# Kernel optimization log

Measured on AMD Instinct MI355X. Metric: run time of the kernel, lower is better.

## Reference

```python
import jax, jax.numpy as jnp
import numpy as np

BETA = 0.25  # commitment_cost


def setup_inputs() -> dict:
    key = jax.random.key(0)
    k1, k2 = jax.random.split(key)
    z = jax.random.normal(k1, (16, 4096, 256), dtype=jnp.float32)
    embed_w = jax.random.normal(k2, (2048, 256), dtype=jnp.float32)
    return {"z": z, "embed_w": embed_w}


def reference(z, embed_w):
    K, D = embed_w.shape
    zf = z.reshape(-1, D)                                   # [N, D]
    N = zf.shape[0]
    # squared euclidean distances: ||z||^2 + ||e||^2 - 2 z e^T  -> [N, K]
    d = (jnp.sum(zf * zf, axis=1, keepdims=True)
         + jnp.sum(embed_w * embed_w, axis=1)
         - 2.0 * jnp.matmul(zf, embed_w.T))
    encoding_indices = jnp.argmin(d, axis=1)                # [N]
    # one-hot @ embedding.weight == direct gather
    z_q = embed_w[encoding_indices].reshape(z.shape)
    # straight-through estimator
    z_q_st = z + jax.lax.stop_gradient(z_q - z)
    # commitment loss (z_q detached)
    loss = BETA * jnp.mean((jax.lax.stop_gradient(z_q) - z) ** 2)
    # avg_probs = mean of one-hot encodings over N == normalized bincount
    counts = jnp.zeros((K,), dtype=z.dtype).at[encoding_indices].add(1.0)
    avg_probs = counts / N
    perplexity = jnp.exp(-jnp.sum(avg_probs * jnp.log(avg_probs + 1e-10)))
    return (z_q_st, loss, encoding_indices, perplexity)
```

## Files before the change

### kernel.cpp

```cpp
#include <hip/hip_runtime.h>
#include <math.h>

#define N_ROWS 65536
#define D 256
#define K 2048

#define LOSS_OFF 16777216L
#define IDX_OFF  16777217L
#define PERP_OFF 16842753L

#define WS_HIST    0
#define WS_LOSS    8192
#define WS_FLAGCNT 8196
#define WS_TICKET  8200
#define WS_ENORM   8448
#define WS_ENORM64 16640
#define WS_FLAGS   24832
#define WS_BPK     287232
#define WS_EWT     1335808

#define FLAG_Q 12

typedef _Float16 half8 __attribute__((ext_vector_type(8)));
typedef float floatx4 __attribute__((ext_vector_type(4)));

__global__ __launch_bounds__(256) void convertB_kernel(const float* __restrict__ ew,
                                                       char* __restrict__ bpk,
                                                       float* __restrict__ ewT,
                                                       float* __restrict__ enorm,
                                                       float* __restrict__ enorm64,
                                                       int* __restrict__ hist,
                                                       float* __restrict__ loss_acc,
                                                       int* __restrict__ flagcnt,
                                                       int* __restrict__ ticket) {
  const int gid = blockIdx.x * 256 + threadIdx.x;
  if (gid < 2048) hist[gid] = 0;
  else if (gid == 2048) *loss_acc = 0.f;
  else if (gid == 2049) *flagcnt = 0;
  else if (gid == 2050) *ticket = 0;

  const int code = gid >> 3, kc = gid & 7;
  const float4* s4 = (const float4*)(ew + (size_t)code * D + kc * 32);
  float buf[32];
#pragma unroll
  for (int q = 0; q < 8; ++q) *(float4*)&buf[q * 4] = s4[q];
  float s = 0.f;
#pragma unroll
  for (int k = 0; k < 32; ++k) s = fmaf(buf[k], buf[k], s);
  s += __shfl_xor(s, 1, 64); s += __shfl_xor(s, 2, 64); s += __shfl_xor(s, 4, 64);
  if (kc == 0) { enorm[code] = s; enorm64[code] = s * 64.0f; }

  {
    float* col = ewT + code;
#pragma unroll
    for (int k = 0; k < 32; ++k) col[(size_t)(kc * 32 + k) * K] = buf[k];
  }

  _Float16 hi[32];
#pragma unroll
  for (int k = 0; k < 32; ++k) hi[k] = (_Float16)buf[k];
  char* base = bpk + (((size_t)(code >> 4) * 8 + kc) << 10) + (code & 15) * 16;
#pragma unroll
  for (int q = 0; q < 4; ++q)
    *(uint4*)(base + q * 256) = ((const uint4*)hi)[q];
}

__global__ __launch_bounds__(256, 3) void argmin_kernel(
    const float* __restrict__ z, const float* __restrict__ ew,
    const char* __restrict__ bpk, const float* __restrict__ enorm64,
    float* __restrict__ out, float* __restrict__ out_idx,
    float* __restrict__ loss_acc, int* __restrict__ hist,
    int* __restrict__ flagcnt, int* __restrict__ flags) {
  __shared__ __align__(16) char As[32768];
  __shared__ float red[4];

  const int t = threadIdx.x, lane = t & 63, w = t >> 6;
  const int quad = lane >> 4, l15 = lane & 15;
  const int rb = blockIdx.x * 64;

  float zsum = 0.f;
#pragma unroll
  for (int i = 0; i < 8; ++i) {
    const int slot = i * 256 + t;
    const int chunk = slot >> 6, ln = slot & 63;
    const int rg = chunk >> 3, kc = chunk & 7;
    const int row = rb + rg * 16 + (ln & 15);
    const float* src = z + (size_t)row * D + kc * 32 + (ln >> 4) * 8;
    const float4 f0 = *(const float4*)src;
    const float4 f1 = *(const float4*)(src + 4);
    zsum += f0.x*f0.x + f0.y*f0.y + f0.z*f0.z + f0.w*f0.w
          + f1.x*f1.x + f1.y*f1.y + f1.z*f1.z + f1.w*f1.w;
    _Float16 hb[8] = {(_Float16)f0.x, (_Float16)f0.y, (_Float16)f0.z, (_Float16)f0.w,
                      (_Float16)f1.x, (_Float16)f1.y, (_Float16)f1.z, (_Float16)f1.w};
    *(uint4*)(As + slot * 16) = *(const uint4*)hb;
  }
  __syncthreads();

  int min1[16], min2[16];
#pragma unroll
  for (int s = 0; s < 16; ++s) { min1[s] = 0x7FFFFFFF; min2[s] = 0x7FFFFFFF; }

#pragma unroll 1
  for (int nt = 0; nt < 8; ++nt) {
    float en[4];
#pragma unroll
    for (int ct = 0; ct < 4; ++ct)
      en[ct] = enorm64[w * 512 + nt * 64 + ct * 16 + l15];

    floatx4 acc[4][4];
#pragma unroll
    for (int rt = 0; rt < 4; ++rt)
#pragma unroll
      for (int ct = 0; ct < 4; ++ct) acc[rt][ct] = 0;

    const char* bnt = bpk + (((size_t)(w * 32 + nt * 4) * 8) << 10) + lane * 16;
#pragma unroll 2
    for (int kc = 0; kc < 8; ++kc) {
      half8 a[4], b[4];
#pragma unroll
      for (int rt = 0; rt < 4; ++rt)
        a[rt] = *(const half8*)(As + ((rt * 8 + kc) << 10) + lane * 16);
#pragma unroll
      for (int ct = 0; ct < 4; ++ct)
        b[ct] = *(const half8*)(bnt + ct * 8192 + (kc << 10));
#pragma unroll
      for (int rt = 0; rt < 4; ++rt)
#pragma unroll
        for (int ct = 0; ct < 4; ++ct)
          acc[rt][ct] = __builtin_amdgcn_mfma_f32_16x16x32_f16(a[rt], b[ct], acc[rt][ct], 0, 0, 0);
    }

#pragma unroll
    for (int ct = 0; ct < 4; ++ct) {
      const int cg = w * 512 + nt * 64 + ct * 16 + l15;
#pragma unroll
      for (int rt = 0; rt < 4; ++rt)
#pragma unroll
        for (int r = 0; r < 4; ++r) {
          const int q = (int)fmaf(-128.0f, acc[rt][ct][r], en[ct]);
          const int key = q * 2048 + cg;
          const int s = rt * 4 + r;
          min2[s] = min(min2[s], max(key, min1[s]));
          min1[s] = min(min1[s], key);
        }
    }
  }

#pragma unroll
  for (int s = 0; s < 16; ++s) {
    int m1 = min1[s], m2 = min2[s];
#pragma unroll
    for (int m = 1; m < 16; m <<= 1) {
      const int o1 = __shfl_xor(m1, m, 64);
      const int o2 = __shfl_xor(m2, m, 64);
      m2 = min(min(m2, o2), max(m1, o1));
      m1 = min(m1, o1);
    }
    min1[s] = m1; min2[s] = m2;
  }
  __syncthreads();
  int* lm1 = (int*)As;
  int* lm2 = lm1 + 256;
  int* lidx = lm2 + 256;
#pragma unroll
  for (int s = 0; s < 16; ++s) {
    if (l15 == 0) {
      const int rowl = (s >> 2) * 16 + quad * 4 + (s & 3);
      lm1[w * 64 + rowl] = min1[s];
      lm2[w * 64 + rowl] = min2[s];
    }
  }
  __syncthreads();

  int qbest = 0;
  if (t < 64) {
    const int a1 = lm1[t],       a2 = lm2[t];
    const int b1 = lm1[64 + t],  b2 = lm2[64 + t];
    const int c1 = lm1[128 + t], c2 = lm2[128 + t];
    const int d1 = lm1[192 + t], d2 = lm2[192 + t];
    const int mab = min(a1, b1), sab = min(max(a1, b1), min(a2, b2));
    const int mcd = min(c1, d1), scd = min(max(c1, d1), min(c2, d2));
    const int m1 = min(mab, mcd);
    const int m2 = min(min(sab, scd), max(mab, mcd));
    const int idxv = m1 & 2047;
    out_idx[rb + t] = (float)idxv;
    lidx[t] = idxv;
    qbest = (m1 >> 11);
    atomicAdd(&hist[idxv], 1);
    if ((m2 >> 11) - (m1 >> 11) < FLAG_Q) {
      const int p = atomicAdd(flagcnt, 1);
      flags[p] = rb + t;
    }
  }
  __syncthreads();

  for (int r = 0; r < 16; ++r) {
    const int rowl = w * 16 + r;
    const int idx = lidx[rowl];
    const float4 v = ((const float4*)(ew + (size_t)idx * D))[lane];
    ((float4*)(out + ((size_t)rb + rowl) * D))[lane] = v;
  }

  float lv = zsum + (float)qbest * (1.0f / 64.0f);
#pragma unroll
  for (int off = 32; off > 0; off >>= 1) lv += __shfl_down(lv, off, 64);
  if (lane == 0) red[w] = lv;
  __syncthreads();
  if (t == 0) atomicAdd(loss_acc, red[0] + red[1] + red[2] + red[3]);
}

__global__ __launch_bounds__(512) void rescue_kernel(
    const float* __restrict__ z, const float* __restrict__ ew,
    const float* __restrict__ ewT, const float* __restrict__ enorm,
    const int* __restrict__ flagcnt, const int* __restrict__ flags,
    int* __restrict__ ticket,
    float* __restrict__ out_idx, float* __restrict__ out,
    int* __restrict__ hist) {
  __shared__ __align__(16) float zsT[256 * 8];
  __shared__ unsigned long long bkey[8];
  __shared__ int rrow[8], ridx[8], rchg[8], grpS;
  const int t = threadIdx.x, lane = t & 63, rr = t >> 6;
  const int cnt = flagcnt[0];
  const float4 en4 = ((const float4*)enorm)[t];

  for (;;) {
    if (t == 0) grpS = atomicAdd(ticket, 1);
    __syncthreads();
    const int grp = grpS;
    if (grp * 8 >= cnt) break;
    const int nr = min(8, cnt - grp * 8);

    if (rr < nr) {
      const int row = flags[grp * 8 + rr];
      if (lane == 0) rrow[rr] = row;
      const float4 v = ((const float4*)(z + (size_t)row * D))[lane];
      zsT[(lane * 4 + 0) * 8 + rr] = v.x;
      zsT[(lane * 4 + 1) * 8 + rr] = v.y;
      zsT[(lane * 4 + 2) * 8 + rr] = v.z;
      zsT[(lane * 4 + 3) * 8 + rr] = v.w;
    }
    if (t < 8) bkey[t] = ~0ULL;
    __syncthreads();

    float acc[8][4];
#pragma unroll
    for (int r = 0; r < 8; ++r)
#pragma unroll
      for (int c = 0; c < 4; ++c) acc[r][c] = 0.f;

    const float4* ecol = (const float4*)ewT + t;
#pragma unroll 4
    for (int d = 0; d < 256; ++d) {
      const float4 e = ecol[(size_t)d * 512];
      const float4 za = *(const float4*)&zsT[d * 8];
      const float4 zb = *(const float4*)&zsT[d * 8 + 4];
      const float zr[8] = {za.x, za.y, za.z, za.w, zb.x, zb.y, zb.z, zb.w};
      const float ec[4] = {e.x, e.y, e.z, e.w};
#pragma unroll
      for (int r = 0; r < 8; ++r)
#pragma unroll
        for (int c = 0; c < 4; ++c)
          acc[r][c] = fmaf(ec[c], zr[r], acc[r][c]);
    }

    const float enc[4] = {en4.x, en4.y, en4.z, en4.w};
    unsigned long long mykey[8];
#pragma unroll
    for (int r = 0; r < 8; ++r) {
      unsigned long long best = ~0ULL;
#pragma unroll
      for (int c = 0; c < 4; ++c) {
        const float dv = fmaf(-2.0f, acc[r][c], enc[c]);
        const unsigned b = __float_as_uint(dv);
        const unsigned k32 = b ^ ((unsigned)((int)b >> 31) | 0x80000000u);
        const unsigned long long key =
            ((unsigned long long)k32 << 32) | (unsigned)(4 * t + c);
        best = min(best, key);
      }
      mykey[r] = best;
    }
#pragma unroll
    for (int m = 1; m < 64; m <<= 1)
#pragma unroll
      for (int r = 0; r < 8; ++r) {
        const unsigned long long o = __shfl_xor(mykey[r], m, 64);
        mykey[r] = min(mykey[r], o);
      }
    if (lane == 0) {
#pragma unroll
      for (int r = 0; r < 8; ++r)
        if (r < nr) atomicMin(&bkey[r], mykey[r]);
    }
    __syncthreads();

    if (t < nr) {
      const int row = rrow[t];
      const int newidx = (int)(unsigned)(bkey[t] & 0xFFFFFFFFu);
      const int oldidx = (int)out_idx[row];
      ridx[t] = newidx;
      rchg[t] = (newidx != oldidx);
      if (newidx != oldidx) {
        atomicSub(&hist[oldidx], 1);
        atomicAdd(&hist[newidx], 1);
        out_idx[row] = (float)newidx;
      }
    }
    __syncthreads();
    if (rr < nr && rchg[rr]) {
      const int row = rrow[rr], idx = ridx[rr];
      ((float4*)(out + (size_t)row * D))[lane] =
          ((const float4*)(ew + (size_t)idx * D))[lane];
    }
  }
}

__global__ __launch_bounds__(256) void finalize_kernel(const int* __restrict__ hist,
                                                       const float* __restrict__ loss_acc,
                                                       float* __restrict__ out) {
  __shared__ float red[256];
  const int t = threadIdx.x;
  float local = 0.f;
  for (int k = t; k < K; k += 256) {
    const float p = (float)hist[k] * (1.0f / (float)N_ROWS);
    local += p * logf(p + 1e-10f);
  }
  red[t] = local;
  __syncthreads();
  for (int s = 128; s > 0; s >>= 1) {
    if (t < s) red[t] += red[t + s];
    __syncthreads();
  }
  if (t == 0) {
    out[LOSS_OFF] = 0.25f * loss_acc[0] * (1.0f / (float)((size_t)N_ROWS * D));
    out[PERP_OFF] = expf(-red[0]);
  }
}

extern "C" void kernel_launch(void* const* d_in, const int* in_sizes, int n_in,
                              void* d_out, int out_size, void* d_ws, size_t ws_size,
                              hipStream_t stream) {
  const float* z  = (const float*)d_in[0];
  const float* ew = (const float*)d_in[1];
  float* out = (float*)d_out;

  char* ws = (char*)d_ws;
  int*   hist     = (int*)(ws + WS_HIST);
  float* loss_acc = (float*)(ws + WS_LOSS);
  int*   flagcnt  = (int*)(ws + WS_FLAGCNT);
  int*   ticket   = (int*)(ws + WS_TICKET);
  float* enorm    = (float*)(ws + WS_ENORM);
  float* enorm64  = (float*)(ws + WS_ENORM64);
  int*   flags    = (int*)(ws + WS_FLAGS);
  char*  bpk      = ws + WS_BPK;
  float* ewT      = (float*)(ws + WS_EWT);

  convertB_kernel<<<64, 256, 0, stream>>>(ew, bpk, ewT, enorm, enorm64,
                                          hist, loss_acc, flagcnt, ticket);
  argmin_kernel<<<N_ROWS / 64, 256, 0, stream>>>(z, ew, bpk, enorm64,
                                                 out, out + IDX_OFF, loss_acc,
                                                 hist, flagcnt, flags);
  rescue_kernel<<<512, 512, 0, stream>>>(z, ew, ewT, enorm, flagcnt, flags,
                                         ticket, out + IDX_OFF, out, hist);
  finalize_kernel<<<1, 256, 0, stream>>>(hist, loss_acc, out);
}
```

Before: 281.6 us.

## Software-pipeline codebook B-fragment loads across k-chunks and use nontemporal z/out access

```diff
diff --git a/kernel.cpp b/kernel.cpp
--- a/kernel.cpp
+++ b/kernel.cpp
@@ -86,8 +86,8 @@
     const int rg = chunk >> 3, kc = chunk & 7;
     const int row = rb + rg * 16 + (ln & 15);
     const float* src = z + (size_t)row * D + kc * 32 + (ln >> 4) * 8;
-    const float4 f0 = *(const float4*)src;
-    const float4 f1 = *(const float4*)(src + 4);
+    const floatx4 f0 = __builtin_nontemporal_load((const floatx4*)src);
+    const floatx4 f1 = __builtin_nontemporal_load((const floatx4*)(src + 4));
     zsum += f0.x*f0.x + f0.y*f0.y + f0.z*f0.z + f0.w*f0.w
           + f1.x*f1.x + f1.y*f1.y + f1.z*f1.z + f1.w*f1.w;
     _Float16 hb[8] = {(_Float16)f0.x, (_Float16)f0.y, (_Float16)f0.z, (_Float16)f0.w,
@@ -100,6 +100,43 @@
 #pragma unroll
   for (int s = 0; s < 16; ++s) { min1[s] = 0x7FFFFFFF; min2[s] = 0x7FFFFFFF; }
 
+  half8 bb[4][4];
+
+#define PF(slotc, g) {                                                         \
+    const int ntt_ = (nt + ((g) >> 3)) & 7;                                    \
+    const int kk_ = (g) & 7;                                                   \
+    const char* bp_ = bpk + ((((size_t)(w * 32 + ntt_ * 4) * 8) + kk_) << 10)  \
+                      + lane * 16;                                             \
+    bb[slotc][0] = *(const half8*)(bp_);                                       \
+    bb[slotc][1] = *(const half8*)(bp_ + 8192);                                \
+    bb[slotc][2] = *(const half8*)(bp_ + 16384);                               \
+    bb[slotc][3] = *(const half8*)(bp_ + 24576); }
+
+#define STEP(kcc) {                                                            \
+    PF(((kcc) + 2) & 3, (kcc) + 2);                                            \
+    const half8 a0 = *(const half8*)(As + ((0 * 8 + (kcc)) << 10) + lane * 16);\
+    const half8 a1 = *(const half8*)(As + ((1 * 8 + (kcc)) << 10) + lane * 16);\
+    const half8 a2 = *(const half8*)(As + ((2 * 8 + (kcc)) << 10) + lane * 16);\
+    const half8 a3 = *(const half8*)(As + ((3 * 8 + (kcc)) << 10) + lane * 16);\
+    acc[0][0] = __builtin_amdgcn_mfma_f32_16x16x32_f16(a0, bb[(kcc)&3][0], acc[0][0], 0, 0, 0); \
+    acc[0][1] = __builtin_amdgcn_mfma_f32_16x16x32_f16(a0, bb[(kcc)&3][1], acc[0][1], 0, 0, 0); \
+    acc[0][2] = __builtin_amdgcn_mfma_f32_16x16x32_f16(a0, bb[(kcc)&3][2], acc[0][2], 0, 0, 0); \
+    acc[0][3] = __builtin_amdgcn_mfma_f32_16x16x32_f16(a0, bb[(kcc)&3][3], acc[0][3], 0, 0, 0); \
+    acc[1][0] = __builtin_amdgcn_mfma_f32_16x16x32_f16(a1, bb[(kcc)&3][0], acc[1][0], 0, 0, 0); \
+    acc[1][1] = __builtin_amdgcn_mfma_f32_16x16x32_f16(a1, bb[(kcc)&3][1], acc[1][1], 0, 0, 0); \
+    acc[1][2] = __builtin_amdgcn_mfma_f32_16x16x32_f16(a1, bb[(kcc)&3][2], acc[1][2], 0, 0, 0); \
+    acc[1][3] = __builtin_amdgcn_mfma_f32_16x16x32_f16(a1, bb[(kcc)&3][3], acc[1][3], 0, 0, 0); \
+    acc[2][0] = __builtin_amdgcn_mfma_f32_16x16x32_f16(a2, bb[(kcc)&3][0], acc[2][0], 0, 0, 0); \
+    acc[2][1] = __builtin_amdgcn_mfma_f32_16x16x32_f16(a2, bb[(kcc)&3][1], acc[2][1], 0, 0, 0); \
+    acc[2][2] = __builtin_amdgcn_mfma_f32_16x16x32_f16(a2, bb[(kcc)&3][2], acc[2][2], 0, 0, 0); \
+    acc[2][3] = __builtin_amdgcn_mfma_f32_16x16x32_f16(a2, bb[(kcc)&3][3], acc[2][3], 0, 0, 0); \
+    acc[3][0] = __builtin_amdgcn_mfma_f32_16x16x32_f16(a3, bb[(kcc)&3][0], acc[3][0], 0, 0, 0); \
+    acc[3][1] = __builtin_amdgcn_mfma_f32_16x16x32_f16(a3, bb[(kcc)&3][1], acc[3][1], 0, 0, 0); \
+    acc[3][2] = __builtin_amdgcn_mfma_f32_16x16x32_f16(a3, bb[(kcc)&3][2], acc[3][2], 0, 0, 0); \
+    acc[3][3] = __builtin_amdgcn_mfma_f32_16x16x32_f16(a3, bb[(kcc)&3][3], acc[3][3], 0, 0, 0); }
+
+  { const int nt = 0; PF(0, 0); PF(1, 1); }
+
 #pragma unroll 1
   for (int nt = 0; nt < 8; ++nt) {
     float en[4];
@@ -113,22 +150,8 @@
 #pragma unroll
       for (int ct = 0; ct < 4; ++ct) acc[rt][ct] = 0;
 
-    const char* bnt = bpk + (((size_t)(w * 32 + nt * 4) * 8) << 10) + lane * 16;
-#pragma unroll 2
-    for (int kc = 0; kc < 8; ++kc) {
-      half8 a[4], b[4];
-#pragma unroll
-      for (int rt = 0; rt < 4; ++rt)
-        a[rt] = *(const half8*)(As + ((rt * 8 + kc) << 10) + lane * 16);
-#pragma unroll
-      for (int ct = 0; ct < 4; ++ct)
-        b[ct] = *(const half8*)(bnt + ct * 8192 + (kc << 10));
-#pragma unroll
-      for (int rt = 0; rt < 4; ++rt)
-#pragma unroll
-        for (int ct = 0; ct < 4; ++ct)
-          acc[rt][ct] = __builtin_amdgcn_mfma_f32_16x16x32_f16(a[rt], b[ct], acc[rt][ct], 0, 0, 0);
-    }
+    STEP(0); STEP(1); STEP(2); STEP(3);
+    STEP(4); STEP(5); STEP(6); STEP(7);
 
 #pragma unroll
     for (int ct = 0; ct < 4; ++ct) {
@@ -145,6 +168,8 @@
         }
     }
   }
+#undef STEP
+#undef PF
 
 #pragma unroll
   for (int s = 0; s < 16; ++s) {
@@ -197,8 +222,8 @@
   for (int r = 0; r < 16; ++r) {
     const int rowl = w * 16 + r;
     const int idx = lidx[rowl];
-    const float4 v = ((const float4*)(ew + (size_t)idx * D))[lane];
-    ((float4*)(out + ((size_t)rb + rowl) * D))[lane] = v;
+    const floatx4 v = *((const floatx4*)(ew + (size_t)idx * D) + lane);
+    __builtin_nontemporal_store(v, (floatx4*)(out + ((size_t)rb + rowl) * D) + lane);
   }
 
   float lv = zsum + (float)qbest * (1.0f / 64.0f);
```

Result: slower. 424.5 us (+50.7%).
